# Kernel optimization log

Hardware: AMD Instinct MI355X
Metric: run time of the kernel (lower is better)

The kernel has to match this reference:

```python
import jax, jax.numpy as jnp
import numpy as np

B, S, D = 2, 2048, 1024
H, DK, DV = 16, 64, 64


def setup_inputs() -> dict:
    key = jax.random.key(0)
    ks = jax.random.split(key, 10)
    scale = 0.02
    return {
        "x": jax.random.normal(ks[0], (B, S, D), dtype=jnp.float32),
        "Wq": jax.random.normal(ks[1], (D, H * DK), dtype=jnp.float32) * scale,
        "bq": jax.random.normal(ks[2], (H * DK,), dtype=jnp.float32) * scale,
        "Wk": jax.random.normal(ks[3], (D, H * DK), dtype=jnp.float32) * scale,
        "bk": jax.random.normal(ks[4], (H * DK,), dtype=jnp.float32) * scale,
        "Wv": jax.random.normal(ks[5], (D, H * DV), dtype=jnp.float32) * scale,
        "bv": jax.random.normal(ks[6], (H * DV,), dtype=jnp.float32) * scale,
        "Wo": jax.random.normal(ks[7], (H * DV, D), dtype=jnp.float32) * scale,
        "bo": jax.random.normal(ks[8], (D,), dtype=jnp.float32) * scale,
    }


def reference(x, Wq, bq, Wk, bk, Wv, bv, Wo, bo):
    b, s, d = x.shape
    # projections -> (b, H, s, dk/dv)
    q = (x @ Wq + bq).reshape(b, s, H, DK).transpose(0, 2, 1, 3)
    k = (x @ Wk + bk).reshape(b, s, H, DK).transpose(0, 2, 1, 3)
    v = (x @ Wv + bv).reshape(b, s, H, DV).transpose(0, 2, 1, 3)
    # scaled QK^T: (b, H, s, s)
    scores = jnp.einsum("bhqd,bhkd->bhqk", q, k) / np.sqrt(DK).astype(np.float32)
    # sign-based reweighting: scores * sign(scores) (zeros -> sign 1) == |scores|
    reweighted = jnp.abs(scores)
    # causal mask: lower triangle keeps value, strict upper -> -inf (value * -inf)
    causal = jnp.tril(jnp.ones((s, s), dtype=bool))
    logits = jnp.where(causal, reweighted, -jnp.inf)
    w = jax.nn.softmax(logits, axis=-1)
    o = jnp.einsum("bhqk,bhkd->bhqd", w, v)  # (b, H, s, DV)
    o = o.transpose(0, 2, 1, 3).reshape(b, s, H * DV)
    return o @ Wo + bo
```

## Files before the change

### kernel.cpp

```cpp
#include <hip/hip_runtime.h>


#define DI __device__ __forceinline__

typedef __bf16 bf16x8 __attribute__((ext_vector_type(8)));
typedef float f32x4 __attribute__((ext_vector_type(4)));
typedef unsigned short u16x8 __attribute__((ext_vector_type(8)));
typedef unsigned short u16x4 __attribute__((ext_vector_type(4)));

union U8 { u16x8 u; bf16x8 b; };
union PB { unsigned int w[4]; u16x8 u; bf16x8 b; };

typedef const __attribute__((address_space(1))) unsigned int* gas_p;
typedef __attribute__((address_space(3))) unsigned int* las_p;

DI void gload16(const unsigned short* g, unsigned short* l) {
  __builtin_amdgcn_global_load_lds((gas_p)(const void*)g, (las_p)(void*)l, 16, 0, 0);
}

#define WAIT_VM4  asm volatile("s_waitcnt vmcnt(4)" ::: "memory")
#define WAIT_VM0  asm volatile("s_waitcnt vmcnt(0)" ::: "memory")
#define WAIT_LGKM asm volatile("s_waitcnt lgkmcnt(0)" ::: "memory")
#define BARRIER   __builtin_amdgcn_s_barrier()

DI unsigned short f2bf(float f) {
  unsigned int u = __float_as_uint(f);
  u += 0x7FFFu + ((u >> 16) & 1u);
  return (unsigned short)(u >> 16);
}
DI float bf2f(unsigned short v) { return __uint_as_float((unsigned int)v << 16); }

__global__ __launch_bounds__(256) void k_conv_x(const float* __restrict__ x,
                                                unsigned short* __restrict__ xb) {
  size_t i = ((size_t)blockIdx.x * 256 + threadIdx.x) * 4;
  float4 v = *(const float4*)(x + i);
  u16x4 o;
  o[0] = f2bf(v.x); o[1] = f2bf(v.y); o[2] = f2bf(v.z); o[3] = f2bf(v.w);
  *(u16x4*)(xb + i) = o;
}

__global__ __launch_bounds__(256) void k_transpose(
    const float* __restrict__ W0, const float* __restrict__ W1,
    const float* __restrict__ W2, const float* __restrict__ W3,
    unsigned short* __restrict__ T0, unsigned short* __restrict__ T1,
    unsigned short* __restrict__ T2, unsigned short* __restrict__ T3) {
  const int z = blockIdx.z;
  const float* W = (z == 0) ? W0 : (z == 1) ? W1 : (z == 2) ? W2 : W3;
  unsigned short* T = (z == 0) ? T0 : (z == 1) ? T1 : (z == 2) ? T2 : T3;
  __shared__ unsigned short buf[32][33];
  const int k0 = blockIdx.x * 32, n0 = blockIdx.y * 32;
  const int tx = threadIdx.x, ty = threadIdx.y;
#pragma unroll
  for (int j = 0; j < 4; ++j) {
    int r = ty + j * 8;
    buf[r][tx] = f2bf(W[(size_t)(k0 + r) * 1024 + n0 + tx]);
  }
  __syncthreads();
#pragma unroll
  for (int j = 0; j < 4; ++j) {
    int c = ty + j * 8;
    T[(size_t)(n0 + c) * 1024 + k0 + tx] = buf[tx][c];
  }
}

DI void stage_gemm(const unsigned short* __restrict__ src, unsigned short* dst,
                   int row0, int k0, int tid, int wid) {
#pragma unroll
  for (int i = 0; i < 2; ++i) {
    int T = i * 256 + tid;
    int row = T >> 2, ch = T & 3;
    int sch = ch ^ (row & 3);
    gload16(&src[(size_t)(row0 + row) * 1024 + k0 + sch * 8],
            &dst[(i * 256 + wid * 64) * 8]);
  }
}

DI void gemm_main(const unsigned short* __restrict__ A,
                  const unsigned short* __restrict__ Bm,
                  unsigned short* As, unsigned short* Bs,
                  int m0, int n0, f32x4 acc[4][4]) {
  const int tid = threadIdx.x;
  const int lane = tid & 63, wid = tid >> 6;
  const int wr = wid >> 1, wc = wid & 1;
  const int g = lane >> 4, lq = lane & 15;

  stage_gemm(A, As, m0, 0, tid, wid);
  stage_gemm(Bm, Bs, n0, 0, tid, wid);
  __syncthreads();
  int buf = 0;
  for (int k0 = 0; k0 < 1024; k0 += 32) {
    if (k0 + 32 < 1024) {
      stage_gemm(A, As + (buf ^ 1) * 4096, m0, k0 + 32, tid, wid);
      stage_gemm(Bm, Bs + (buf ^ 1) * 4096, n0, k0 + 32, tid, wid);
    }
    const unsigned short* Ab = As + buf * 4096;
    const unsigned short* Bb = Bs + buf * 4096;
    U8 af[4], bfr[4];
#pragma unroll
    for (int f = 0; f < 4; ++f) {
      af[f].u  = *(const u16x8*)&Ab[(wr * 64 + f * 16 + lq) * 32 + ((g ^ (lq & 3)) * 8)];
      bfr[f].u = *(const u16x8*)&Bb[(wc * 64 + f * 16 + lq) * 32 + ((g ^ (lq & 3)) * 8)];
    }
#pragma unroll
    for (int i = 0; i < 4; ++i)
#pragma unroll
      for (int j = 0; j < 4; ++j)
        acc[i][j] = __builtin_amdgcn_mfma_f32_16x16x32_bf16(af[i].b, bfr[j].b,
                                                            acc[i][j], 0, 0, 0);
    __syncthreads();
    buf ^= 1;
  }
}

__global__ __launch_bounds__(256) void k_gemm_qkv(
    const unsigned short* __restrict__ xb,
    const unsigned short* __restrict__ Wqt, const unsigned short* __restrict__ Wkt,
    const unsigned short* __restrict__ Wvt,
    const float* __restrict__ bq, const float* __restrict__ bk,
    const float* __restrict__ bv,
    unsigned short* __restrict__ Qo, unsigned short* __restrict__ Ko,
    unsigned short* __restrict__ Vto) {
  __shared__ unsigned short Sh[128 * 136];
  unsigned short* As = Sh;
  unsigned short* Bs = Sh + 8192;
  const int z = blockIdx.z;
  const unsigned short* Bm = (z == 0) ? Wqt : (z == 1) ? Wkt : Wvt;
  const float* bias = (z == 0) ? bq : (z == 1) ? bk : bv;

  f32x4 acc[4][4];
#pragma unroll
  for (int i = 0; i < 4; ++i)
#pragma unroll
    for (int j = 0; j < 4; ++j) acc[i][j] = f32x4{0.f, 0.f, 0.f, 0.f};

  const int m0 = blockIdx.x * 128, n0 = blockIdx.y * 128;
  gemm_main(xb, Bm, As, Bs, m0, n0, acc);

  const int tid = threadIdx.x;
  const int lane = tid & 63, wid = tid >> 6;
  const int wr = wid >> 1, wc = wid & 1;
  const int g = lane >> 4, lq = lane & 15;
  const int bb = m0 >> 11;

#pragma unroll
  for (int j = 0; j < 4; ++j) {
    int col = wc * 64 + j * 16 + lq;
    float bv_ = bias[n0 + col];
#pragma unroll
    for (int i = 0; i < 4; ++i)
#pragma unroll
      for (int r = 0; r < 4; ++r) {
        int row = wr * 64 + i * 16 + g * 4 + r;
        Sh[row * 136 + col] = f2bf(acc[i][j][r] + bv_);
      }
  }
  __syncthreads();

  if (z < 2) {
    unsigned short* dstQK = (z == 0) ? Qo : Ko;
    const int ch = tid & 15, sb = tid >> 4;
#pragma unroll
    for (int it = 0; it < 8; ++it) {
      int s = sb + it * 16;
      u16x8 v = *(const u16x8*)&Sh[s * 136 + ch * 8];
      int gcol = n0 + ch * 8;
      int hh = gcol >> 6, dd = gcol & 63;
      int sr = (m0 + s) & 2047;
      *(u16x8*)&dstQK[(((size_t)(bb * 16 + hh)) * 2048 + sr) * 64 + dd] = v;
    }
  } else {
    const int d = tid & 127, hf = tid >> 7;
    int gcol = n0 + d;
    int hh = gcol >> 6, dd = gcol & 63;
    size_t vrow = ((size_t)(bb * 16 + hh)) * 64 + dd;
#pragma unroll
    for (int it = 0; it < 8; ++it) {
      int s0 = (hf + it * 2) * 8;
      u16x8 vv;
#pragma unroll
      for (int e = 0; e < 8; ++e) vv[e] = Sh[(s0 + e) * 136 + d];
      *(u16x8*)&Vto[vrow * 2048 + (m0 & 2047) + s0] = vv;
    }
  }
}

__global__ __launch_bounds__(256) void k_gemm_out(
    const unsigned short* __restrict__ Ob, const unsigned short* __restrict__ Wot,
    const float* __restrict__ bo, float* __restrict__ out) {
  __shared__ unsigned short As[2 * 4096];
  __shared__ unsigned short Bs[2 * 4096];
  f32x4 acc[4][4];
#pragma unroll
  for (int i = 0; i < 4; ++i)
#pragma unroll
    for (int j = 0; j < 4; ++j) acc[i][j] = f32x4{0.f, 0.f, 0.f, 0.f};

  const int m0 = blockIdx.x * 128, n0 = blockIdx.y * 128;
  gemm_main(Ob, Wot, As, Bs, m0, n0, acc);

  const int lane = threadIdx.x & 63, wid = threadIdx.x >> 6;
  const int wr = wid >> 1, wc = wid & 1;
  const int g = lane >> 4, lq = lane & 15;
#pragma unroll
  for (int j = 0; j < 4; ++j) {
    int col = n0 + wc * 64 + j * 16 + lq;
    float bv_ = bo[col];
#pragma unroll
    for (int i = 0; i < 4; ++i)
#pragma unroll
      for (int r = 0; r < 4; ++r) {
        int row = m0 + wr * 64 + i * 16 + g * 4 + r;
        out[(size_t)row * 1024 + col] = acc[i][j][r] + bv_;
      }
  }
}

template<bool MASKED>
DI void ptile(f32x4 sacc[4], f32x4& lacc, unsigned int pk[4][2],
              int qrow, int kk0, int g) {
  const float SC = 0.18033688011112042f;
#pragma unroll
  for (int c = 0; c < 4; ++c) {
#pragma unroll
    for (int r = 0; r < 4; ++r) {
      float sv = fabsf(sacc[c][r]) * SC;
      if (MASKED) {
        int k = kk0 + g * 8 + r + 4 * (c & 1) + 32 * (c >> 1);
        sv = (k <= qrow) ? sv : -1e30f;
      }
      float p = exp2f(sv);
      sacc[c][r] = p;
      lacc[r] += p;
    }
    asm("v_cvt_pk_bf16_f32 %0, %1, %2"
        : "=v"(pk[c][0]) : "v"(sacc[c][0]), "v"(sacc[c][1]));
    asm("v_cvt_pk_bf16_f32 %0, %1, %2"
        : "=v"(pk[c][1]) : "v"(sacc[c][2]), "v"(sacc[c][3]));
  }
}

DI void flash_dual(bool complete, int qblk, int t0, int t1, int slot,
                   const unsigned short* __restrict__ Q,
                   const unsigned short* __restrict__ Km,
                   const unsigned short* __restrict__ Vt,
                   unsigned short* __restrict__ O,
                   unsigned short* __restrict__ Pp, float* __restrict__ Lp,
                   unsigned short* Ks0, unsigned short* Vs0,
                   size_t qkbase, size_t vbase, int b, int h,
                   int tid, int wid, int g, int lq) {
  const int lrowA = wid * 32 + lq, lrowB = lrowA + 16;
  const int qrowA = qblk * 128 + lrowA, qrowB = qblk * 128 + lrowB;
  const int diag0 = 2 * qblk;

  auto stage = [&](int bf, int t) {
    const int kk0 = t * 64;
#pragma unroll
    for (int i = 0; i < 2; ++i) {
      int T = i * 256 + tid;
      int row = T >> 3, ch = T & 7;
      int sch = ch ^ (row & 7);
      gload16(&Km[qkbase + (size_t)(kk0 + row) * 64 + sch * 8],
              Ks0 + bf * 4096 + (i * 2048 + wid * 512));
      gload16(&Vt[vbase + (size_t)row * 2048 + kk0 + sch * 8],
              Vs0 + bf * 4096 + (i * 2048 + wid * 512));
    }
  };

  U8 aqA0, aqA1, aqB0, aqB1;
  {
    const unsigned short* qp = &Q[qkbase + (size_t)qrowA * 64 + g * 8];
    aqA0.u = *(const u16x8*)qp;
    aqA1.u = *(const u16x8*)(qp + 32);
    const unsigned short* qp2 = &Q[qkbase + (size_t)qrowB * 64 + g * 8];
    aqB0.u = *(const u16x8*)qp2;
    aqB1.u = *(const u16x8*)(qp2 + 32);
  }
  f32x4 laccA = f32x4{0.f, 0.f, 0.f, 0.f}, laccB = f32x4{0.f, 0.f, 0.f, 0.f};
  f32x4 oaccA[4], oaccB[4];
#pragma unroll
  for (int c = 0; c < 4; ++c) {
    oaccA[c] = f32x4{0.f, 0.f, 0.f, 0.f};
    oaccB[c] = f32x4{0.f, 0.f, 0.f, 0.f};
  }

  const int rbase = (lq >> 2) * 8 + (lq & 3);

  stage(0, t0);
  if (t0 + 1 < t1) stage(1, t0 + 1);
  int buf = 0;
  for (int t = t0; t < t1; ++t) {
    if (t + 1 < t1) WAIT_VM4; else WAIT_VM0;
    BARRIER;
    const unsigned short* Kb = Ks0 + buf * 4096;
    const unsigned short* Vb = Vs0 + buf * 4096;
    const int kk0 = t * 64;
    f32x4 saccA[4], saccB[4];
    __builtin_amdgcn_s_setprio(1);
#pragma unroll
    for (int c = 0; c < 4; ++c) {
      int row = rbase + 4 * (c & 1) + 32 * (c >> 1);
      int r7 = row & 7;
      U8 kf0, kf1;
      kf0.u = *(const u16x8*)&Kb[row * 64 + ((g ^ r7) * 8)];
      kf1.u = *(const u16x8*)&Kb[row * 64 + (((4 + g) ^ r7) * 8)];
      saccA[c] = __builtin_amdgcn_mfma_f32_16x16x32_bf16(kf0.b, aqA0.b,
                                                         f32x4{0.f, 0.f, 0.f, 0.f}, 0, 0, 0);
      saccA[c] = __builtin_amdgcn_mfma_f32_16x16x32_bf16(kf1.b, aqA1.b, saccA[c], 0, 0, 0);
      saccB[c] = __builtin_amdgcn_mfma_f32_16x16x32_bf16(kf0.b, aqB0.b,
                                                         f32x4{0.f, 0.f, 0.f, 0.f}, 0, 0, 0);
      saccB[c] = __builtin_amdgcn_mfma_f32_16x16x32_bf16(kf1.b, aqB1.b, saccB[c], 0, 0, 0);
    }
    __builtin_amdgcn_s_setprio(0);
    unsigned int pkA[4][2], pkB[4][2];
    if (t >= diag0) {
      ptile<true>(saccA, laccA, pkA, qrowA, kk0, g);
      ptile<true>(saccB, laccB, pkB, qrowB, kk0, g);
    } else {
      ptile<false>(saccA, laccA, pkA, qrowA, kk0, g);
      ptile<false>(saccB, laccB, pkB, qrowB, kk0, g);
    }
    __builtin_amdgcn_s_setprio(1);
#pragma unroll
    for (int hh = 0; hh < 2; ++hh) {
      PB pbA, pbB;
      pbA.w[0] = pkA[hh * 2 + 0][0]; pbA.w[1] = pkA[hh * 2 + 0][1];
      pbA.w[2] = pkA[hh * 2 + 1][0]; pbA.w[3] = pkA[hh * 2 + 1][1];
      pbB.w[0] = pkB[hh * 2 + 0][0]; pbB.w[1] = pkB[hh * 2 + 0][1];
      pbB.w[2] = pkB[hh * 2 + 1][0]; pbB.w[3] = pkB[hh * 2 + 1][1];
#pragma unroll
      for (int c = 0; c < 4; ++c) {
        U8 vf;
        vf.u = *(const u16x8*)&Vb[(c * 16 + lq) * 64 + (((hh * 4 + g) ^ (lq & 7)) * 8)];
        oaccA[c] = __builtin_amdgcn_mfma_f32_16x16x32_bf16(vf.b, pbA.b, oaccA[c], 0, 0, 0);
        oaccB[c] = __builtin_amdgcn_mfma_f32_16x16x32_bf16(vf.b, pbB.b, oaccB[c], 0, 0, 0);
      }
    }
    __builtin_amdgcn_s_setprio(0);
    WAIT_LGKM;
    BARRIER;
    if (t + 2 < t1) stage(buf, t + 2);
    buf ^= 1;
  }

  float lsA = (laccA[0] + laccA[1]) + (laccA[2] + laccA[3]);
  lsA += __shfl_xor(lsA, 16, 64);
  lsA += __shfl_xor(lsA, 32, 64);
  float lsB = (laccB[0] + laccB[1]) + (laccB[2] + laccB[3]);
  lsB += __shfl_xor(lsB, 16, 64);
  lsB += __shfl_xor(lsB, 32, 64);
  if (complete) {
    float invA = 1.0f / lsA, invB = 1.0f / lsB;
#pragma unroll
    for (int c = 0; c < 4; ++c) {
      u16x4 ovA, ovB;
#pragma unroll
      for (int r2 = 0; r2 < 4; ++r2) {
        ovA[r2] = f2bf(oaccA[c][r2] * invA);
        ovB[r2] = f2bf(oaccB[c][r2] * invB);
      }
      *(u16x4*)&O[((size_t)(b * 2048 + qrowA)) * 1024 + h * 64 + c * 16 + g * 4] = ovA;
      *(u16x4*)&O[((size_t)(b * 2048 + qrowB)) * 1024 + h * 64 + c * 16 + g * 4] = ovB;
    }
  } else {
    if (g == 0) {
      Lp[slot * 128 + lrowA] = lsA;
      Lp[slot * 128 + lrowB] = lsB;
    }
    size_t pbase = (size_t)slot * 8192;
#pragma unroll
    for (int c = 0; c < 4; ++c) {
      u16x4 ovA, ovB;
#pragma unroll
      for (int r2 = 0; r2 < 4; ++r2) {
        ovA[r2] = f2bf(oaccA[c][r2]);
        ovB[r2] = f2bf(oaccB[c][r2]);
      }
      *(u16x4*)&Pp[pbase + lrowA * 64 + c * 16 + g * 4] = ovA;
      *(u16x4*)&Pp[pbase + lrowB * 64 + c * 16 + g * 4] = ovB;
    }
  }
}

__global__ __launch_bounds__(256) void k_flash(
    const unsigned short* __restrict__ Q, const unsigned short* __restrict__ Km,
    const unsigned short* __restrict__ Vt, unsigned short* __restrict__ O,
    unsigned short* __restrict__ Pp, float* __restrict__ Lp) {
  __shared__ unsigned short Ks[2 * 4096];
  __shared__ unsigned short Vs[2 * 4096];
  const int tid = threadIdx.x;
  const int lane = tid & 63, wid = tid >> 6;
  const int g = lane >> 4, lq = lane & 15;
  const int bid = blockIdx.x;
  const int xcd = bid & 7, idx = bid >> 3;
  const int bh = xcd * 4 + (idx >> 4);
  const int rr = idx & 15;
  const int p = rr >> 1, sp = rr & 1;
  const int mp = 15 - p;
  const int b = bh >> 4, h = bh & 15;
  const size_t qkbase = (size_t)bh * 2048 * 64;
  const size_t vbase = (size_t)bh * 64 * 2048;

  if (sp == 0) {
    flash_dual(true, p, 0, 2 * p + 2, 0, Q, Km, Vt, O, Pp, Lp,
               Ks, Vs, qkbase, vbase, b, h, tid, wid, g, lq);
    flash_dual(false, mp, 0, 15 - 2 * p, (bh * 8 + p) * 2 + 0, Q, Km, Vt, O, Pp, Lp,
               Ks, Vs, qkbase, vbase, b, h, tid, wid, g, lq);
  } else {
    flash_dual(false, mp, 15 - 2 * p, 32 - 2 * p, (bh * 8 + p) * 2 + 1, Q, Km, Vt, O, Pp, Lp,
               Ks, Vs, qkbase, vbase, b, h, tid, wid, g, lq);
  }
}

__global__ __launch_bounds__(256) void k_combine(
    const unsigned short* __restrict__ Pp, const float* __restrict__ Lp,
    unsigned short* __restrict__ O) {
  int gid = blockIdx.x * 256 + threadIdx.x;
  int dv4 = gid & 15;
  int q   = (gid >> 4) & 127;
  int pi  = (gid >> 11) & 7;
  int bh  = gid >> 14;
  int slot0 = (bh * 8 + pi) * 2;
  size_t base = (size_t)slot0 * 8192 + q * 64 + dv4 * 4;
  u16x4 a = *(const u16x4*)&Pp[base];
  u16x4 c = *(const u16x4*)&Pp[base + 8192];
  float l = Lp[slot0 * 128 + q] + Lp[(slot0 + 1) * 128 + q];
  float inv = 1.0f / l;
  u16x4 o;
#pragma unroll
  for (int r = 0; r < 4; ++r) o[r] = f2bf((bf2f(a[r]) + bf2f(c[r])) * inv);
  int b = bh >> 4, h = bh & 15;
  int srow = (15 - pi) * 128 + q;
  *(u16x4*)&O[((size_t)(b * 2048 + srow)) * 1024 + h * 64 + dv4 * 4] = o;
}

extern "C" void kernel_launch(void* const* d_in, const int* in_sizes, int n_in,
                              void* d_out, int out_size, void* d_ws, size_t ws_size,
                              hipStream_t stream) {
  const float* x  = (const float*)d_in[0];
  const float* Wq = (const float*)d_in[1];
  const float* bq = (const float*)d_in[2];
  const float* Wk = (const float*)d_in[3];
  const float* bk = (const float*)d_in[4];
  const float* Wv = (const float*)d_in[5];
  const float* bv = (const float*)d_in[6];
  const float* Wo = (const float*)d_in[7];
  const float* bo = (const float*)d_in[8];
  float* out = (float*)d_out;

  char* ws = (char*)d_ws;
  const size_t MB = 1024 * 1024;
  unsigned short* xb   = (unsigned short*)(ws + 0 * MB);
  unsigned short* Wqt  = (unsigned short*)(ws + 8 * MB);
  unsigned short* Wkt  = (unsigned short*)(ws + 10 * MB);
  unsigned short* Wvt  = (unsigned short*)(ws + 12 * MB);
  unsigned short* Wot  = (unsigned short*)(ws + 14 * MB);
  unsigned short* Qws  = (unsigned short*)(ws + 16 * MB);
  unsigned short* Kws  = (unsigned short*)(ws + 24 * MB);
  unsigned short* Vtws = (unsigned short*)(ws + 32 * MB);
  unsigned short* Ows  = (unsigned short*)(ws + 40 * MB);
  unsigned short* Pp   = (unsigned short*)(ws + 0 * MB);
  float*          Lp   = (float*)(ws + 8 * MB);

  k_conv_x<<<4096, 256, 0, stream>>>(x, xb);
  k_transpose<<<dim3(32, 32, 4), dim3(32, 8), 0, stream>>>(Wq, Wk, Wv, Wo,
                                                           Wqt, Wkt, Wvt, Wot);
  k_gemm_qkv<<<dim3(32, 8, 3), 256, 0, stream>>>(xb, Wqt, Wkt, Wvt, bq, bk, bv,
                                                 Qws, Kws, Vtws);
  k_flash<<<512, 256, 0, stream>>>(Qws, Kws, Vtws, Ows, Pp, Lp);
  k_combine<<<2048, 256, 0, stream>>>(Pp, Lp, Ows);
  k_gemm_out<<<dim3(32, 8), 256, 0, stream>>>(Ows, Wot, bo, out);
}
```

Baseline: 111.1 us.

## Halve flash query tile to 64 rows with 128-thread blocks and doubled grid

Shrinks the attention query block from 128 to 64 rows, runs 2 waves per block instead of 4, and launches 1024 blocks instead of 512. The causal pairing and split scheme, the staging loop (4 iterations per thread), the vmcnt wait depth, the diagonal test and the combine indexing are all rewritten for 64-row tiles. The aim is finer load balance and more resident blocks for the causal workload. In exchange each K/V tile staged into LDS is reused by fewer query rows, so K/V traffic per unit of work roughly doubles.

```diff
diff --git a/kernel.cpp b/kernel.cpp
--- a/kernel.cpp
+++ b/kernel.cpp
@@ -18,7 +18,7 @@
   __builtin_amdgcn_global_load_lds((gas_p)(const void*)g, (las_p)(void*)l, 16, 0, 0);
 }
 
-#define WAIT_VM4  asm volatile("s_waitcnt vmcnt(4)" ::: "memory")
+#define WAIT_VM8  asm volatile("s_waitcnt vmcnt(8)" ::: "memory")
 #define WAIT_VM0  asm volatile("s_waitcnt vmcnt(0)" ::: "memory")
 #define WAIT_LGKM asm volatile("s_waitcnt lgkmcnt(0)" ::: "memory")
 #define BARRIER   __builtin_amdgcn_s_barrier()
@@ -249,20 +249,19 @@
                    size_t qkbase, size_t vbase, int b, int h,
                    int tid, int wid, int g, int lq) {
   const int lrowA = wid * 32 + lq, lrowB = lrowA + 16;
-  const int qrowA = qblk * 128 + lrowA, qrowB = qblk * 128 + lrowB;
-  const int diag0 = 2 * qblk;
+  const int qrowA = qblk * 64 + lrowA, qrowB = qblk * 64 + lrowB;
 
   auto stage = [&](int bf, int t) {
     const int kk0 = t * 64;
 #pragma unroll
-    for (int i = 0; i < 2; ++i) {
-      int T = i * 256 + tid;
+    for (int i = 0; i < 4; ++i) {
+      int T = i * 128 + tid;
       int row = T >> 3, ch = T & 7;
       int sch = ch ^ (row & 7);
       gload16(&Km[qkbase + (size_t)(kk0 + row) * 64 + sch * 8],
-              Ks0 + bf * 4096 + (i * 2048 + wid * 512));
+              Ks0 + bf * 4096 + (i * 1024 + wid * 512));
       gload16(&Vt[vbase + (size_t)row * 2048 + kk0 + sch * 8],
-              Vs0 + bf * 4096 + (i * 2048 + wid * 512));
+              Vs0 + bf * 4096 + (i * 1024 + wid * 512));
     }
   };
 
@@ -289,7 +288,7 @@
   if (t0 + 1 < t1) stage(1, t0 + 1);
   int buf = 0;
   for (int t = t0; t < t1; ++t) {
-    if (t + 1 < t1) WAIT_VM4; else WAIT_VM0;
+    if (t + 1 < t1) WAIT_VM8; else WAIT_VM0;
     BARRIER;
     const unsigned short* Kb = Ks0 + buf * 4096;
     const unsigned short* Vb = Vs0 + buf * 4096;
@@ -312,7 +311,7 @@
     }
     __builtin_amdgcn_s_setprio(0);
     unsigned int pkA[4][2], pkB[4][2];
-    if (t >= diag0) {
+    if (t == qblk) {
       ptile<true>(saccA, laccA, pkA, qrowA, kk0, g);
       ptile<true>(saccB, laccB, pkB, qrowB, kk0, g);
     } else {
@@ -363,10 +362,10 @@
     }
   } else {
     if (g == 0) {
-      Lp[slot * 128 + lrowA] = lsA;
-      Lp[slot * 128 + lrowB] = lsB;
-    }
-    size_t pbase = (size_t)slot * 8192;
+      Lp[slot * 64 + lrowA] = lsA;
+      Lp[slot * 64 + lrowB] = lsB;
+    }
+    size_t pbase = (size_t)slot * 4096;
 #pragma unroll
     for (int c = 0; c < 4; ++c) {
       u16x4 ovA, ovB;
@@ -381,7 +380,7 @@
   }
 }
 
-__global__ __launch_bounds__(256) void k_flash(
+__global__ __launch_bounds__(128) void k_flash(
     const unsigned short* __restrict__ Q, const unsigned short* __restrict__ Km,
     const unsigned short* __restrict__ Vt, unsigned short* __restrict__ O,
     unsigned short* __restrict__ Pp, float* __restrict__ Lp) {
@@ -391,22 +390,22 @@
   const int lane = tid & 63, wid = tid >> 6;
   const int g = lane >> 4, lq = lane & 15;
   const int bid = blockIdx.x;
-  const int xcd = bid & 7, idx = bid >> 3;
-  const int bh = xcd * 4 + (idx >> 4);
-  const int rr = idx & 15;
+  const int xcd = bid & 7, r = bid >> 3;
+  const int bh = xcd * 4 + (r >> 5);
+  const int rr = r & 31;
   const int p = rr >> 1, sp = rr & 1;
-  const int mp = 15 - p;
+  const int mq = 31 - p, mi = 15 - p;
   const int b = bh >> 4, h = bh & 15;
   const size_t qkbase = (size_t)bh * 2048 * 64;
   const size_t vbase = (size_t)bh * 64 * 2048;
 
   if (sp == 0) {
-    flash_dual(true, p, 0, 2 * p + 2, 0, Q, Km, Vt, O, Pp, Lp,
+    flash_dual(true, p, 0, p + 1, 0, Q, Km, Vt, O, Pp, Lp,
                Ks, Vs, qkbase, vbase, b, h, tid, wid, g, lq);
-    flash_dual(false, mp, 0, 15 - 2 * p, (bh * 8 + p) * 2 + 0, Q, Km, Vt, O, Pp, Lp,
+    flash_dual(false, mq, 0, 16 - p, (bh * 16 + mi) * 2 + 0, Q, Km, Vt, O, Pp, Lp,
                Ks, Vs, qkbase, vbase, b, h, tid, wid, g, lq);
   } else {
-    flash_dual(false, mp, 15 - 2 * p, 32 - 2 * p, (bh * 8 + p) * 2 + 1, Q, Km, Vt, O, Pp, Lp,
+    flash_dual(false, mq, 16 - p, 32 - p, (bh * 16 + mi) * 2 + 1, Q, Km, Vt, O, Pp, Lp,
                Ks, Vs, qkbase, vbase, b, h, tid, wid, g, lq);
   }
 }
@@ -416,20 +415,20 @@
     unsigned short* __restrict__ O) {
   int gid = blockIdx.x * 256 + threadIdx.x;
   int dv4 = gid & 15;
-  int q   = (gid >> 4) & 127;
-  int pi  = (gid >> 11) & 7;
+  int q   = (gid >> 4) & 63;
+  int mi  = (gid >> 10) & 15;
   int bh  = gid >> 14;
-  int slot0 = (bh * 8 + pi) * 2;
-  size_t base = (size_t)slot0 * 8192 + q * 64 + dv4 * 4;
+  int pairbase = (bh * 16 + mi) * 2;
+  size_t base = (size_t)pairbase * 4096 + q * 64 + dv4 * 4;
   u16x4 a = *(const u16x4*)&Pp[base];
-  u16x4 c = *(const u16x4*)&Pp[base + 8192];
-  float l = Lp[slot0 * 128 + q] + Lp[(slot0 + 1) * 128 + q];
+  u16x4 c = *(const u16x4*)&Pp[base + 4096];
+  float l = Lp[pairbase * 64 + q] + Lp[(pairbase + 1) * 64 + q];
   float inv = 1.0f / l;
   u16x4 o;
 #pragma unroll
   for (int r = 0; r < 4; ++r) o[r] = f2bf((bf2f(a[r]) + bf2f(c[r])) * inv);
   int b = bh >> 4, h = bh & 15;
-  int srow = (15 - pi) * 128 + q;
+  int srow = (mi + 16) * 64 + q;
   *(u16x4*)&O[((size_t)(b * 2048 + srow)) * 1024 + h * 64 + dv4 * 4] = o;
 }
 
@@ -466,7 +465,7 @@
                                                            Wqt, Wkt, Wvt, Wot);
   k_gemm_qkv<<<dim3(32, 8, 3), 256, 0, stream>>>(xb, Wqt, Wkt, Wvt, bq, bk, bv,
                                                  Qws, Kws, Vtws);
-  k_flash<<<512, 256, 0, stream>>>(Qws, Kws, Vtws, Ows, Pp, Lp);
+  k_flash<<<1024, 128, 0, stream>>>(Qws, Kws, Vtws, Ows, Pp, Lp);
   k_combine<<<2048, 256, 0, stream>>>(Pp, Lp, Ows);
   k_gemm_out<<<dim3(32, 8), 256, 0, stream>>>(Ows, Wot, bo, out);
 }
```

After: 114.8 us. +3.3%, slower.
